# Optimization experiments

Measured on AMD Instinct MI355X. Metric: run time of the kernel, lower is better.

Reference implementation:

```python
import jax, jax.numpy as jnp
import numpy as np

N_NODES = 100000


def gcn_conv(x, src, dst, w, W, b, n):
    # PyG GCNConv: add self loops (weight 1), symmetric normalization,
    # linear transform, scatter-add aggregation, bias.
    loop = jnp.arange(n, dtype=src.dtype)
    s = jnp.concatenate([src, loop])
    d = jnp.concatenate([dst, loop])
    ew = jnp.concatenate([w, jnp.ones((n,), dtype=w.dtype)])
    deg = jax.ops.segment_sum(ew, d, num_segments=n)          # [N]
    dinv = jnp.where(deg > 0, jax.lax.rsqrt(deg), 0.0).astype(x.dtype)
    norm = dinv[s] * ew * dinv[d]                             # [E+N]
    h = x @ W                                                 # [N, out]
    msg = h[s] * norm[:, None]                                # gather + scale
    out = jax.ops.segment_sum(msg, d, num_segments=n)         # scatter-add
    return out + b


def setup_inputs() -> dict:
    key = jax.random.key(0)
    k1, k2, k3, k4, k5, k6 = jax.random.split(key, 6)
    n, e, c_in, c_hid, c_out = N_NODES, 1200000, 64, 64, 32
    node_matrix = jax.random.normal(k1, (n, c_in), dtype=jnp.float32)
    edge_index = jax.random.randint(k2, (2, e), 0, n, dtype=jnp.int64)
    edge_weights = jax.random.uniform(k3, (e,), dtype=jnp.float32)
    s_in = 1.0 / np.sqrt(c_in)
    s_hid = 1.0 / np.sqrt(c_hid)
    W1 = jax.random.uniform(k4, (c_in, c_hid), jnp.float32, -s_in, s_in)
    b1 = jnp.zeros((c_hid,), jnp.float32)
    W2 = jax.random.uniform(k5, (c_hid, c_out), jnp.float32, -s_hid, s_hid)
    b2 = jnp.zeros((c_out,), jnp.float32)
    return {"node_matrix": node_matrix, "edge_index": edge_index,
            "edge_weights": edge_weights, "W1": W1, "b1": b1, "W2": W2, "b2": b2}


def reference(node_matrix, edge_index, edge_weights, W1, b1, W2, b2):
    n = node_matrix.shape[0]
    src, dst = edge_index[0], edge_index[1]
    x = gcn_conv(node_matrix, src, dst, edge_weights, W1, b1, n)
    x = jax.nn.relu(x)
    x = gcn_conv(x, src, dst, edge_weights, W2, b2, n)
    return x
```

## Files before the change

kernel.cpp:

```cpp
#include <hip/hip_runtime.h>

static inline int ceil_div(long long a, long long b) { return (int)((a + b - 1) / b); }

#define RBITS 8
#define RNODES 256
#define CNT_BLOCKS 96

typedef __attribute__((ext_vector_type(8))) short bf16x8;
typedef __attribute__((ext_vector_type(4))) float f32x4;

__device__ inline unsigned f2bf(float f) {
    unsigned u = __float_as_uint(f);
    return (u + 0x7fffu + ((u >> 16) & 1u)) >> 16;
}
__device__ inline unsigned pack2(float a, float b) { return f2bf(a) | (f2bf(b) << 16); }
__device__ inline float bf2f(unsigned v) { return __uint_as_float(v << 16); }
__device__ inline float bf_lo(unsigned v) { return __uint_as_float(v << 16); }
__device__ inline float bf_hi(unsigned v) { return __uint_as_float(v & 0xffff0000u); }

__global__ void bin_count(const int* __restrict__ dst, int* __restrict__ hist_g,
                          int NB, int E) {
    __shared__ int hist[512];
    int t = threadIdx.x;
    hist[t] = 0;
    __syncthreads();
    int nvec = E >> 2;
    const int4* d4 = (const int4*)dst;
    for (int v = blockIdx.x * 512 + t; v < nvec; v += CNT_BLOCKS * 512) {
        int4 d = d4[v];
        atomicAdd(&hist[d.x >> RBITS], 1);
        atomicAdd(&hist[d.y >> RBITS], 1);
        atomicAdd(&hist[d.z >> RBITS], 1);
        atomicAdd(&hist[d.w >> RBITS], 1);
    }
    if (blockIdx.x == 0 && t < (E & 3))
        atomicAdd(&hist[dst[(nvec << 2) + t] >> RBITS], 1);
    __syncthreads();
    if (t < NB) hist_g[blockIdx.x * NB + t] = hist[t];
}

__global__ void bin_scan(const int* __restrict__ hist_g, int* __restrict__ bin_start,
                         int* __restrict__ bin_cursor, int NB) {
    __shared__ int s[512];
    int t = threadIdx.x;
    int v = 0;
    if (t < NB) {
        for (int k = 0; k < CNT_BLOCKS; ++k) v += hist_g[k * NB + t];
        bin_cursor[t] = 0;
    }
    s[t] = v;
    __syncthreads();
    for (int d = 1; d < 512; d <<= 1) {
        int a = (t >= d) ? s[t - d] : 0;
        __syncthreads();
        s[t] += a;
        __syncthreads();
    }
    if (t < NB) bin_start[t] = s[t] - v;
    if (t == NB - 1) bin_start[NB] = s[t];
}

#define SC_T 512
#define SC_K 8
#define SC_E (SC_T * SC_K)
__global__ void bin_scatter(const int* __restrict__ src, const int* __restrict__ dst,
                            const float* __restrict__ w, int* __restrict__ bin_cursor,
                            const int* __restrict__ bin_start,
                            int* __restrict__ bp, float* __restrict__ bw,
                            int NB, int E) {
    __shared__ int hist[512];
    __shared__ int offs[512];
    __shared__ int base[512];
    __shared__ int stage_p[SC_E];
    __shared__ float stage_w[SC_E];
    __shared__ unsigned short stage_b[SC_E];
    int t = threadIdx.x;
    hist[t] = 0;
    __syncthreads();
    int e0 = blockIdx.x * SC_E;
    int nE = E - e0; if (nE > SC_E) nE = SC_E;

    int myBin[SC_K], myRank[SC_K], myPack[SC_K];
    float myW[SC_K];
#pragma unroll
    for (int k = 0; k < SC_K; ++k) {
        int idx = t + k * SC_T;
        if (idx < nE) {
            int e = e0 + idx;
            int d = dst[e];
            int b = d >> RBITS;
            myBin[k] = b;
            myPack[k] = (src[e] << RBITS) | (d & (RNODES - 1));
            myW[k] = w[e];
            myRank[k] = atomicAdd(&hist[b], 1);
        }
    }
    __syncthreads();
    offs[t] = hist[t];
    __syncthreads();
    for (int d = 1; d < 512; d <<= 1) {
        int a = (t >= d) ? offs[t - d] : 0;
        __syncthreads();
        offs[t] += a;
        __syncthreads();
    }
    if (t < NB && hist[t]) base[t] = bin_start[t] + atomicAdd(&bin_cursor[t], hist[t]);
#pragma unroll
    for (int k = 0; k < SC_K; ++k) {
        int idx = t + k * SC_T;
        if (idx < nE) {
            int b = myBin[k];
            int pos = (offs[b] - hist[b]) + myRank[k];
            stage_p[pos] = myPack[k];
            stage_w[pos] = myW[k];
            stage_b[pos] = (unsigned short)b;
        }
    }
    __syncthreads();
    for (int p = t; p < nE; p += SC_T) {
        int b = stage_b[p];
        int g = base[b] + (p - (offs[b] - hist[b]));
        bp[g] = stage_p[p];
        bw[g] = stage_w[p];
    }
}

__global__ void deg_csr(const int* __restrict__ bp, const float* __restrict__ bw,
                        const int* __restrict__ bin_start,
                        int* __restrict__ row_beg, int* __restrict__ row_cnt,
                        float* __restrict__ dinv, int N) {
    __shared__ int cnt[RNODES];
    __shared__ float wsum[RNODES];
    __shared__ int starts[RNODES];
    int b = blockIdx.x;
    int t = threadIdx.x;
    if (t < RNODES) { cnt[t] = 0; wsum[t] = 0.f; }
    __syncthreads();
    int beg = bin_start[b], end = bin_start[b + 1];
    for (int e = beg + t; e < end; e += 512) {
        int off = bp[e] & (RNODES - 1);
        atomicAdd(&cnt[off], 1);
        atomicAdd(&wsum[off], bw[e]);
    }
    __syncthreads();
    if (t < RNODES) starts[t] = cnt[t];
    __syncthreads();
    for (int d = 1; d < RNODES; d <<= 1) {
        int a = 0;
        if (t < RNODES && t >= d) a = starts[t - d];
        __syncthreads();
        if (t < RNODES) starts[t] += a;
        __syncthreads();
    }
    if (t < RNODES) {
        int node = (b << RBITS) + t;
        if (node < N) {
            row_beg[node] = beg + (starts[t] - cnt[t]);
            row_cnt[node] = cnt[t];
            dinv[node] = rsqrtf(wsum[t] + 1.0f);
        }
    }
}

__global__ void csr_scatter(const int* __restrict__ bp, const float* __restrict__ bw,
                            const int* __restrict__ bin_start, const int* __restrict__ row_beg,
                            const float* __restrict__ dinv, uint2* __restrict__ ew, int N) {
    __shared__ int cur[RNODES];
    int b = blockIdx.x;
    int t = threadIdx.x;
    if (t < RNODES) {
        int node = (b << RBITS) + t;
        cur[t] = (node < N) ? row_beg[node] : 0;
    }
    __syncthreads();
    int beg = bin_start[b], end = bin_start[b + 1];
    for (int e = beg + t; e < end; e += 512) {
        int p = bp[e];
        int s = p >> RBITS;
        int slot = atomicAdd(&cur[p & (RNODES - 1)], 1);
        uint2 v;
        v.x = (unsigned)s;
        v.y = __float_as_uint(bw[e] * dinv[s]);
        ew[slot] = v;
    }
}

__global__ __launch_bounds__(256) void gemm1_mfma(const float* __restrict__ X,
                                                  const float* __restrict__ W,
                                                  unsigned short* __restrict__ H, int N) {
    int lane = threadIdx.x & 63;
    int wv = threadIdx.x >> 6;
    int quad = lane >> 4;
    int col = lane & 15;

    bf16x8 Bh[4][2], Bl[4][2];
#pragma unroll
    for (int nt = 0; nt < 4; ++nt)
#pragma unroll
        for (int kh = 0; kh < 2; ++kh)
#pragma unroll
            for (int j = 0; j < 8; ++j) {
                float wval = W[(kh * 32 + quad * 8 + j) * 64 + nt * 16 + col];
                unsigned hb = f2bf(wval);
                Bh[nt][kh][j] = (short)hb;
                Bl[nt][kh][j] = (short)f2bf(wval - bf2f(hb));
            }

#pragma unroll
    for (int rt = 0; rt < 4; ++rt) {
        int rb = blockIdx.x * 256 + wv * 64 + rt * 16;
        if (rb >= N) break;
        int arow = rb + col;
        bf16x8 Ah[2], Al[2];
#pragma unroll
        for (int kh = 0; kh < 2; ++kh) {
            float xv[8];
            if (arow < N) {
                const float4* p = (const float4*)(X + (size_t)arow * 64 + kh * 32 + quad * 8);
                float4 f0 = p[0], f1 = p[1];
                xv[0] = f0.x; xv[1] = f0.y; xv[2] = f0.z; xv[3] = f0.w;
                xv[4] = f1.x; xv[5] = f1.y; xv[6] = f1.z; xv[7] = f1.w;
            } else {
#pragma unroll
                for (int j = 0; j < 8; ++j) xv[j] = 0.f;
            }
#pragma unroll
            for (int j = 0; j < 8; ++j) {
                unsigned hb = f2bf(xv[j]);
                Ah[kh][j] = (short)hb;
                Al[kh][j] = (short)f2bf(xv[j] - bf2f(hb));
            }
        }
        f32x4 acc[4] = {{0,0,0,0},{0,0,0,0},{0,0,0,0},{0,0,0,0}};
#pragma unroll
        for (int nt = 0; nt < 4; ++nt)
#pragma unroll
            for (int kh = 0; kh < 2; ++kh) {
                acc[nt] = __builtin_amdgcn_mfma_f32_16x16x32_bf16(Ah[kh], Bh[nt][kh], acc[nt], 0, 0, 0);
                acc[nt] = __builtin_amdgcn_mfma_f32_16x16x32_bf16(Al[kh], Bh[nt][kh], acc[nt], 0, 0, 0);
                acc[nt] = __builtin_amdgcn_mfma_f32_16x16x32_bf16(Ah[kh], Bl[nt][kh], acc[nt], 0, 0, 0);
            }
#pragma unroll
        for (int nt = 0; nt < 4; ++nt)
#pragma unroll
            for (int r = 0; r < 4; ++r) {
                int row = rb + quad * 4 + r;
                if (row < N)
                    H[(size_t)row * 64 + nt * 16 + col] = (unsigned short)f2bf(acc[nt][r]);
            }
    }
}

__global__ __launch_bounds__(256) void gemm2_mfma(const unsigned short* __restrict__ Xb,
                                                  const float* __restrict__ W,
                                                  unsigned short* __restrict__ H, int N) {
    int lane = threadIdx.x & 63;
    int wv = threadIdx.x >> 6;
    int quad = lane >> 4;
    int col = lane & 15;

    bf16x8 Bh[2][2], Bl[2][2];
#pragma unroll
    for (int nt = 0; nt < 2; ++nt)
#pragma unroll
        for (int kh = 0; kh < 2; ++kh)
#pragma unroll
            for (int j = 0; j < 8; ++j) {
                float wval = W[(kh * 32 + quad * 8 + j) * 32 + nt * 16 + col];
                unsigned hb = f2bf(wval);
                Bh[nt][kh][j] = (short)hb;
                Bl[nt][kh][j] = (short)f2bf(wval - bf2f(hb));
            }

#pragma unroll
    for (int rt = 0; rt < 4; ++rt) {
        int rb = blockIdx.x * 256 + wv * 64 + rt * 16;
        if (rb >= N) break;
        int arow = rb + col;
        bf16x8 A[2];
#pragma unroll
        for (int kh = 0; kh < 2; ++kh) {
            if (arow < N) {
                const bf16x8* p = (const bf16x8*)(Xb + (size_t)arow * 64 + kh * 32 + quad * 8);
                A[kh] = *p;
            } else {
                A[kh] = bf16x8{0,0,0,0,0,0,0,0};
            }
        }
        f32x4 acc[2] = {{0,0,0,0},{0,0,0,0}};
#pragma unroll
        for (int nt = 0; nt < 2; ++nt)
#pragma unroll
            for (int kh = 0; kh < 2; ++kh) {
                acc[nt] = __builtin_amdgcn_mfma_f32_16x16x32_bf16(A[kh], Bh[nt][kh], acc[nt], 0, 0, 0);
                acc[nt] = __builtin_amdgcn_mfma_f32_16x16x32_bf16(A[kh], Bl[nt][kh], acc[nt], 0, 0, 0);
            }
#pragma unroll
        for (int nt = 0; nt < 2; ++nt)
#pragma unroll
            for (int r = 0; r < 4; ++r) {
                int row = rb + quad * 4 + r;
                if (row < N)
                    H[(size_t)row * 32 + nt * 16 + col] = (unsigned short)f2bf(acc[nt][r]);
            }
    }
}

__global__ void aggregate64(const unsigned* __restrict__ h, const int* __restrict__ row_beg,
                            const int* __restrict__ row_cnt, const uint2* __restrict__ ew,
                            const float* __restrict__ dinv, const float* __restrict__ b,
                            unsigned* __restrict__ outb, int N) {
    int t = threadIdx.x;
    int c = t & 7;
    int i = blockIdx.x * 64 + (t >> 3);
    if (i >= N) return;
    int e = row_beg[i];
    int end = e + row_cnt[i];
    const uint4* h4 = (const uint4*)h;
    float acc[8];
#pragma unroll
    for (int j = 0; j < 8; ++j) acc[j] = 0.f;
    for (; e + 3 < end; e += 4) {
        uint2 e0 = ew[e], e1 = ew[e + 1], e2 = ew[e + 2], e3 = ew[e + 3];
        float n0 = __uint_as_float(e0.y);
        float n1 = __uint_as_float(e1.y);
        float n2 = __uint_as_float(e2.y);
        float n3 = __uint_as_float(e3.y);
        uint4 v0 = h4[(size_t)e0.x * 8 + c];
        uint4 v1 = h4[(size_t)e1.x * 8 + c];
        uint4 v2 = h4[(size_t)e2.x * 8 + c];
        uint4 v3 = h4[(size_t)e3.x * 8 + c];
        acc[0] += n0 * bf_lo(v0.x) + n1 * bf_lo(v1.x) + n2 * bf_lo(v2.x) + n3 * bf_lo(v3.x);
        acc[1] += n0 * bf_hi(v0.x) + n1 * bf_hi(v1.x) + n2 * bf_hi(v2.x) + n3 * bf_hi(v3.x);
        acc[2] += n0 * bf_lo(v0.y) + n1 * bf_lo(v1.y) + n2 * bf_lo(v2.y) + n3 * bf_lo(v3.y);
        acc[3] += n0 * bf_hi(v0.y) + n1 * bf_hi(v1.y) + n2 * bf_hi(v2.y) + n3 * bf_hi(v3.y);
        acc[4] += n0 * bf_lo(v0.z) + n1 * bf_lo(v1.z) + n2 * bf_lo(v2.z) + n3 * bf_lo(v3.z);
        acc[5] += n0 * bf_hi(v0.z) + n1 * bf_hi(v1.z) + n2 * bf_hi(v2.z) + n3 * bf_hi(v3.z);
        acc[6] += n0 * bf_lo(v0.w) + n1 * bf_lo(v1.w) + n2 * bf_lo(v2.w) + n3 * bf_lo(v3.w);
        acc[7] += n0 * bf_hi(v0.w) + n1 * bf_hi(v1.w) + n2 * bf_hi(v2.w) + n3 * bf_hi(v3.w);
    }
    for (; e < end; ++e) {
        uint2 e0 = ew[e];
        float n0 = __uint_as_float(e0.y);
        uint4 v0 = h4[(size_t)e0.x * 8 + c];
        acc[0] += n0 * bf_lo(v0.x);
        acc[1] += n0 * bf_hi(v0.x);
        acc[2] += n0 * bf_lo(v0.y);
        acc[3] += n0 * bf_hi(v0.y);
        acc[4] += n0 * bf_lo(v0.z);
        acc[5] += n0 * bf_hi(v0.z);
        acc[6] += n0 * bf_lo(v0.w);
        acc[7] += n0 * bf_hi(v0.w);
    }
    float di = dinv[i];
    uint4 hv = h4[(size_t)i * 8 + c];
    float hs[8] = {bf_lo(hv.x), bf_hi(hv.x), bf_lo(hv.y), bf_hi(hv.y),
                   bf_lo(hv.z), bf_hi(hv.z), bf_lo(hv.w), bf_hi(hv.w)};
    float4 b0 = ((const float4*)b)[c * 2];
    float4 b1 = ((const float4*)b)[c * 2 + 1];
    float o[8];
    o[0] = b0.x + di * (di * hs[0] + acc[0]);
    o[1] = b0.y + di * (di * hs[1] + acc[1]);
    o[2] = b0.z + di * (di * hs[2] + acc[2]);
    o[3] = b0.w + di * (di * hs[3] + acc[3]);
    o[4] = b1.x + di * (di * hs[4] + acc[4]);
    o[5] = b1.y + di * (di * hs[5] + acc[5]);
    o[6] = b1.z + di * (di * hs[6] + acc[6]);
    o[7] = b1.w + di * (di * hs[7] + acc[7]);
#pragma unroll
    for (int j = 0; j < 8; ++j) o[j] = fmaxf(o[j], 0.f);
    uint4 ov;
    ov.x = pack2(o[0], o[1]);
    ov.y = pack2(o[2], o[3]);
    ov.z = pack2(o[4], o[5]);
    ov.w = pack2(o[6], o[7]);
    ((uint4*)outb)[(size_t)i * 8 + c] = ov;
}

__global__ void aggregate32(const unsigned* __restrict__ h, const int* __restrict__ row_beg,
                            const int* __restrict__ row_cnt, const uint2* __restrict__ ew,
                            const float* __restrict__ dinv, const float* __restrict__ b,
                            float* __restrict__ out, int N) {
    int t = threadIdx.x;
    int c = t & 3;
    int i = blockIdx.x * 128 + (t >> 2);
    if (i >= N) return;
    int e = row_beg[i];
    int end = e + row_cnt[i];
    const uint4* h4 = (const uint4*)h;
    float acc[8];
#pragma unroll
    for (int j = 0; j < 8; ++j) acc[j] = 0.f;
    for (; e + 3 < end; e += 4) {
        uint2 e0 = ew[e], e1 = ew[e + 1], e2 = ew[e + 2], e3 = ew[e + 3];
        float n0 = __uint_as_float(e0.y);
        float n1 = __uint_as_float(e1.y);
        float n2 = __uint_as_float(e2.y);
        float n3 = __uint_as_float(e3.y);
        uint4 v0 = h4[(size_t)e0.x * 4 + c];
        uint4 v1 = h4[(size_t)e1.x * 4 + c];
        uint4 v2 = h4[(size_t)e2.x * 4 + c];
        uint4 v3 = h4[(size_t)e3.x * 4 + c];
        acc[0] += n0 * bf_lo(v0.x) + n1 * bf_lo(v1.x) + n2 * bf_lo(v2.x) + n3 * bf_lo(v3.x);
        acc[1] += n0 * bf_hi(v0.x) + n1 * bf_hi(v1.x) + n2 * bf_hi(v2.x) + n3 * bf_hi(v3.x);
        acc[2] += n0 * bf_lo(v0.y) + n1 * bf_lo(v1.y) + n2 * bf_lo(v2.y) + n3 * bf_lo(v3.y);
        acc[3] += n0 * bf_hi(v0.y) + n1 * bf_hi(v1.y) + n2 * bf_hi(v2.y) + n3 * bf_hi(v3.y);
        acc[4] += n0 * bf_lo(v0.z) + n1 * bf_lo(v1.z) + n2 * bf_lo(v2.z) + n3 * bf_lo(v3.z);
        acc[5] += n0 * bf_hi(v0.z) + n1 * bf_hi(v1.z) + n2 * bf_hi(v2.z) + n3 * bf_hi(v3.z);
        acc[6] += n0 * bf_lo(v0.w) + n1 * bf_lo(v1.w) + n2 * bf_lo(v2.w) + n3 * bf_lo(v3.w);
        acc[7] += n0 * bf_hi(v0.w) + n1 * bf_hi(v1.w) + n2 * bf_hi(v2.w) + n3 * bf_hi(v3.w);
    }
    for (; e < end; ++e) {
        uint2 e0 = ew[e];
        float n0 = __uint_as_float(e0.y);
        uint4 v0 = h4[(size_t)e0.x * 4 + c];
        acc[0] += n0 * bf_lo(v0.x);
        acc[1] += n0 * bf_hi(v0.x);
        acc[2] += n0 * bf_lo(v0.y);
        acc[3] += n0 * bf_hi(v0.y);
        acc[4] += n0 * bf_lo(v0.z);
        acc[5] += n0 * bf_hi(v0.z);
        acc[6] += n0 * bf_lo(v0.w);
        acc[7] += n0 * bf_hi(v0.w);
    }
    float di = dinv[i];
    uint4 hv = h4[(size_t)i * 4 + c];
    float hs[8] = {bf_lo(hv.x), bf_hi(hv.x), bf_lo(hv.y), bf_hi(hv.y),
                   bf_lo(hv.z), bf_hi(hv.z), bf_lo(hv.w), bf_hi(hv.w)};
    float4 b0 = ((const float4*)b)[c * 2];
    float4 b1 = ((const float4*)b)[c * 2 + 1];
    float4 o0, o1;
    o0.x = b0.x + di * (di * hs[0] + acc[0]);
    o0.y = b0.y + di * (di * hs[1] + acc[1]);
    o0.z = b0.z + di * (di * hs[2] + acc[2]);
    o0.w = b0.w + di * (di * hs[3] + acc[3]);
    o1.x = b1.x + di * (di * hs[4] + acc[4]);
    o1.y = b1.y + di * (di * hs[5] + acc[5]);
    o1.z = b1.z + di * (di * hs[6] + acc[6]);
    o1.w = b1.w + di * (di * hs[7] + acc[7]);
    float4* op = (float4*)(out + (size_t)i * 32 + c * 8);
    op[0] = o0;
    op[1] = o1;
}

extern "C" void kernel_launch(void* const* d_in, const int* in_sizes, int n_in,
                              void* d_out, int out_size, void* d_ws, size_t ws_size,
                              hipStream_t stream) {
    const float* x  = (const float*)d_in[0];
    const int* eidx = (const int*)d_in[1];
    const float* w  = (const float*)d_in[2];
    const float* W1 = (const float*)d_in[3];
    const float* b1 = (const float*)d_in[4];
    const float* W2 = (const float*)d_in[5];
    const float* b2 = (const float*)d_in[6];
    float* out = (float*)d_out;

    const int E = in_sizes[2];
    const int N = in_sizes[0] / 64;
    const int* src = eidx;
    const int* dst = eidx + E;
    const int NB = ceil_div(N, RNODES);

    char* ws = (char*)d_ws;
    size_t off = 0;
    auto alloc = [&](size_t bytes) -> void* {
        void* p = ws + off;
        off = (off + bytes + 255) & ~(size_t)255;
        return p;
    };
    int*      hist_g     = (int*)alloc((size_t)CNT_BLOCKS * NB * 4);
    int*      bin_cursor = (int*)alloc((size_t)NB * 4);
    int*      bin_start  = (int*)alloc((size_t)(NB + 1) * 4);
    int*      bp         = (int*)alloc((size_t)E * 4);
    float*    bw         = (float*)alloc((size_t)E * 4);
    uint2*    ew         = (uint2*)alloc((size_t)E * 8);
    int*      row_beg    = (int*)alloc((size_t)N * 4);
    int*      row_cnt    = (int*)alloc((size_t)N * 4);
    float*    dinv       = (float*)alloc((size_t)N * 4);
    unsigned* h1         = (unsigned*)alloc((size_t)N * 32 * 4);
    unsigned* out1b      = (unsigned*)alloc((size_t)N * 32 * 4);
    unsigned* h2         = (unsigned*)alloc((size_t)N * 16 * 4);

    bin_count<<<CNT_BLOCKS, 512, 0, stream>>>(dst, hist_g, NB, E);
    bin_scan<<<1, 512, 0, stream>>>(hist_g, bin_start, bin_cursor, NB);
    bin_scatter<<<ceil_div(E, SC_E), SC_T, 0, stream>>>(src, dst, w, bin_cursor, bin_start,
                                                        bp, bw, NB, E);
    deg_csr<<<NB, 512, 0, stream>>>(bp, bw, bin_start, row_beg, row_cnt, dinv, N);
    csr_scatter<<<NB, 512, 0, stream>>>(bp, bw, bin_start, row_beg, dinv, ew, N);

    gemm1_mfma<<<ceil_div(N, 256), 256, 0, stream>>>(x, W1, (unsigned short*)h1, N);
    aggregate64<<<ceil_div(N, 64), 512, 0, stream>>>(h1, row_beg, row_cnt, ew, dinv, b1, out1b, N);

    gemm2_mfma<<<ceil_div(N, 256), 256, 0, stream>>>((const unsigned short*)out1b, W2,
                                                     (unsigned short*)h2, N);
    aggregate32<<<ceil_div(N, 128), 512, 0, stream>>>(h2, row_beg, row_cnt, ew, dinv, b2, out, N);
}
```

Before: 201.9 us.

## Fold source dinv into GEMM output, pack edges to 4 bytes, merge CSR kernels

The source-side degree normalization now happens in the GEMM epilogue (h scaled by dinv per row). Each CSR edge entry then only needs the raw weight, packed with the source index into one 32-bit word (17-bit index, 15-bit bf16 weight). The degree/CSR-offset kernel and the CSR scatter kernel are merged into one, staging the bin's edges in shared memory so they are read from global memory once. This halves edge-list traffic in both aggregation passes and drops a launch. In exchange, edge weights lose precision to truncated bf16 and node indices are limited to 17 bits.

```diff
diff --git a/kernel.cpp b/kernel.cpp
--- a/kernel.cpp
+++ b/kernel.cpp
@@ -5,6 +5,7 @@
 #define RBITS 8
 #define RNODES 256
 #define CNT_BLOCKS 96
+#define STAGE_CAP 4096
 
 typedef __attribute__((ext_vector_type(8))) short bf16x8;
 typedef __attribute__((ext_vector_type(4))) float f32x4;
@@ -125,22 +126,28 @@
     }
 }
 
-__global__ void deg_csr(const int* __restrict__ bp, const float* __restrict__ bw,
-                        const int* __restrict__ bin_start,
-                        int* __restrict__ row_beg, int* __restrict__ row_cnt,
-                        float* __restrict__ dinv, int N) {
+__global__ void csr_build(const int* __restrict__ bp, const float* __restrict__ bw,
+                          const int* __restrict__ bin_start,
+                          int* __restrict__ row_beg, int* __restrict__ row_cnt,
+                          float* __restrict__ dinv, unsigned* __restrict__ ew, int N) {
     __shared__ int cnt[RNODES];
     __shared__ float wsum[RNODES];
     __shared__ int starts[RNODES];
+    __shared__ int cur[RNODES];
+    __shared__ int sp[STAGE_CAP];
+    __shared__ float sw[STAGE_CAP];
     int b = blockIdx.x;
     int t = threadIdx.x;
     if (t < RNODES) { cnt[t] = 0; wsum[t] = 0.f; }
     __syncthreads();
     int beg = bin_start[b], end = bin_start[b + 1];
-    for (int e = beg + t; e < end; e += 512) {
-        int off = bp[e] & (RNODES - 1);
-        atomicAdd(&cnt[off], 1);
-        atomicAdd(&wsum[off], bw[e]);
+    int n = end - beg;
+    for (int idx = t; idx < n; idx += 512) {
+        int p = bp[beg + idx];
+        float wv = bw[beg + idx];
+        if (idx < STAGE_CAP) { sp[idx] = p; sw[idx] = wv; }
+        atomicAdd(&cnt[p & (RNODES - 1)], 1);
+        atomicAdd(&wsum[p & (RNODES - 1)], wv);
     }
     __syncthreads();
     if (t < RNODES) starts[t] = cnt[t];
@@ -153,40 +160,29 @@
         __syncthreads();
     }
     if (t < RNODES) {
+        int ex = starts[t] - cnt[t];
+        cur[t] = beg + ex;
         int node = (b << RBITS) + t;
         if (node < N) {
-            row_beg[node] = beg + (starts[t] - cnt[t]);
+            row_beg[node] = beg + ex;
             row_cnt[node] = cnt[t];
             dinv[node] = rsqrtf(wsum[t] + 1.0f);
         }
     }
-}
-
-__global__ void csr_scatter(const int* __restrict__ bp, const float* __restrict__ bw,
-                            const int* __restrict__ bin_start, const int* __restrict__ row_beg,
-                            const float* __restrict__ dinv, uint2* __restrict__ ew, int N) {
-    __shared__ int cur[RNODES];
-    int b = blockIdx.x;
-    int t = threadIdx.x;
-    if (t < RNODES) {
-        int node = (b << RBITS) + t;
-        cur[t] = (node < N) ? row_beg[node] : 0;
-    }
-    __syncthreads();
-    int beg = bin_start[b], end = bin_start[b + 1];
-    for (int e = beg + t; e < end; e += 512) {
-        int p = bp[e];
-        int s = p >> RBITS;
+    __syncthreads();
+    for (int idx = t; idx < n; idx += 512) {
+        int p;
+        float wv;
+        if (idx < STAGE_CAP) { p = sp[idx]; wv = sw[idx]; }
+        else { p = bp[beg + idx]; wv = bw[beg + idx]; }
         int slot = atomicAdd(&cur[p & (RNODES - 1)], 1);
-        uint2 v;
-        v.x = (unsigned)s;
-        v.y = __float_as_uint(bw[e] * dinv[s]);
-        ew[slot] = v;
+        ew[slot] = ((unsigned)(p >> RBITS) << 15) | (f2bf(wv) & 0x7fffu);
     }
 }
 
 __global__ __launch_bounds__(256) void gemm1_mfma(const float* __restrict__ X,
                                                   const float* __restrict__ W,
+                                                  const float* __restrict__ dinv,
                                                   unsigned short* __restrict__ H, int N) {
     int lane = threadIdx.x & 63;
     int wv = threadIdx.x >> 6;
@@ -240,19 +236,26 @@
                 acc[nt] = __builtin_amdgcn_mfma_f32_16x16x32_bf16(Al[kh], Bh[nt][kh], acc[nt], 0, 0, 0);
                 acc[nt] = __builtin_amdgcn_mfma_f32_16x16x32_bf16(Ah[kh], Bl[nt][kh], acc[nt], 0, 0, 0);
             }
+        float dval[4];
+#pragma unroll
+        for (int r = 0; r < 4; ++r) {
+            int row = rb + quad * 4 + r;
+            dval[r] = (row < N) ? dinv[row] : 0.f;
+        }
 #pragma unroll
         for (int nt = 0; nt < 4; ++nt)
 #pragma unroll
             for (int r = 0; r < 4; ++r) {
                 int row = rb + quad * 4 + r;
                 if (row < N)
-                    H[(size_t)row * 64 + nt * 16 + col] = (unsigned short)f2bf(acc[nt][r]);
+                    H[(size_t)row * 64 + nt * 16 + col] = (unsigned short)f2bf(acc[nt][r] * dval[r]);
             }
     }
 }
 
 __global__ __launch_bounds__(256) void gemm2_mfma(const unsigned short* __restrict__ Xb,
                                                   const float* __restrict__ W,
+                                                  const float* __restrict__ dinv,
                                                   unsigned short* __restrict__ H, int N) {
     int lane = threadIdx.x & 63;
     int wv = threadIdx.x >> 6;
@@ -295,19 +298,25 @@
                 acc[nt] = __builtin_amdgcn_mfma_f32_16x16x32_bf16(A[kh], Bh[nt][kh], acc[nt], 0, 0, 0);
                 acc[nt] = __builtin_amdgcn_mfma_f32_16x16x32_bf16(A[kh], Bl[nt][kh], acc[nt], 0, 0, 0);
             }
+        float dval[4];
+#pragma unroll
+        for (int r = 0; r < 4; ++r) {
+            int row = rb + quad * 4 + r;
+            dval[r] = (row < N) ? dinv[row] : 0.f;
+        }
 #pragma unroll
         for (int nt = 0; nt < 2; ++nt)
 #pragma unroll
             for (int r = 0; r < 4; ++r) {
                 int row = rb + quad * 4 + r;
                 if (row < N)
-                    H[(size_t)row * 32 + nt * 16 + col] = (unsigned short)f2bf(acc[nt][r]);
-            }
-    }
-}
-
-__global__ void aggregate64(const unsigned* __restrict__ h, const int* __restrict__ row_beg,
-                            const int* __restrict__ row_cnt, const uint2* __restrict__ ew,
+                    H[(size_t)row * 32 + nt * 16 + col] = (unsigned short)f2bf(acc[nt][r] * dval[r]);
+            }
+    }
+}
+
+__global__ void aggregate64(const unsigned* __restrict__ g, const int* __restrict__ row_beg,
+                            const int* __restrict__ row_cnt, const unsigned* __restrict__ ew,
                             const float* __restrict__ dinv, const float* __restrict__ b,
                             unsigned* __restrict__ outb, int N) {
     int t = threadIdx.x;
@@ -316,20 +325,20 @@
     if (i >= N) return;
     int e = row_beg[i];
     int end = e + row_cnt[i];
-    const uint4* h4 = (const uint4*)h;
+    const uint4* h4 = (const uint4*)g;
     float acc[8];
 #pragma unroll
     for (int j = 0; j < 8; ++j) acc[j] = 0.f;
     for (; e + 3 < end; e += 4) {
-        uint2 e0 = ew[e], e1 = ew[e + 1], e2 = ew[e + 2], e3 = ew[e + 3];
-        float n0 = __uint_as_float(e0.y);
-        float n1 = __uint_as_float(e1.y);
-        float n2 = __uint_as_float(e2.y);
-        float n3 = __uint_as_float(e3.y);
-        uint4 v0 = h4[(size_t)e0.x * 8 + c];
-        uint4 v1 = h4[(size_t)e1.x * 8 + c];
-        uint4 v2 = h4[(size_t)e2.x * 8 + c];
-        uint4 v3 = h4[(size_t)e3.x * 8 + c];
+        unsigned e0 = ew[e], e1 = ew[e + 1], e2 = ew[e + 2], e3 = ew[e + 3];
+        float n0 = __uint_as_float((e0 & 0x7fffu) << 16);
+        float n1 = __uint_as_float((e1 & 0x7fffu) << 16);
+        float n2 = __uint_as_float((e2 & 0x7fffu) << 16);
+        float n3 = __uint_as_float((e3 & 0x7fffu) << 16);
+        uint4 v0 = h4[(size_t)(e0 >> 15) * 8 + c];
+        uint4 v1 = h4[(size_t)(e1 >> 15) * 8 + c];
+        uint4 v2 = h4[(size_t)(e2 >> 15) * 8 + c];
+        uint4 v3 = h4[(size_t)(e3 >> 15) * 8 + c];
         acc[0] += n0 * bf_lo(v0.x) + n1 * bf_lo(v1.x) + n2 * bf_lo(v2.x) + n3 * bf_lo(v3.x);
         acc[1] += n0 * bf_hi(v0.x) + n1 * bf_hi(v1.x) + n2 * bf_hi(v2.x) + n3 * bf_hi(v3.x);
         acc[2] += n0 * bf_lo(v0.y) + n1 * bf_lo(v1.y) + n2 * bf_lo(v2.y) + n3 * bf_lo(v3.y);
@@ -340,9 +349,9 @@
         acc[7] += n0 * bf_hi(v0.w) + n1 * bf_hi(v1.w) + n2 * bf_hi(v2.w) + n3 * bf_hi(v3.w);
     }
     for (; e < end; ++e) {
-        uint2 e0 = ew[e];
-        float n0 = __uint_as_float(e0.y);
-        uint4 v0 = h4[(size_t)e0.x * 8 + c];
+        unsigned e0 = ew[e];
+        float n0 = __uint_as_float((e0 & 0x7fffu) << 16);
+        uint4 v0 = h4[(size_t)(e0 >> 15) * 8 + c];
         acc[0] += n0 * bf_lo(v0.x);
         acc[1] += n0 * bf_hi(v0.x);
         acc[2] += n0 * bf_lo(v0.y);
@@ -359,14 +368,14 @@
     float4 b0 = ((const float4*)b)[c * 2];
     float4 b1 = ((const float4*)b)[c * 2 + 1];
     float o[8];
-    o[0] = b0.x + di * (di * hs[0] + acc[0]);
-    o[1] = b0.y + di * (di * hs[1] + acc[1]);
-    o[2] = b0.z + di * (di * hs[2] + acc[2]);
-    o[3] = b0.w + di * (di * hs[3] + acc[3]);
-    o[4] = b1.x + di * (di * hs[4] + acc[4]);
-    o[5] = b1.y + di * (di * hs[5] + acc[5]);
-    o[6] = b1.z + di * (di * hs[6] + acc[6]);
-    o[7] = b1.w + di * (di * hs[7] + acc[7]);
+    o[0] = b0.x + di * (hs[0] + acc[0]);
+    o[1] = b0.y + di * (hs[1] + acc[1]);
+    o[2] = b0.z + di * (hs[2] + acc[2]);
+    o[3] = b0.w + di * (hs[3] + acc[3]);
+    o[4] = b1.x + di * (hs[4] + acc[4]);
+    o[5] = b1.y + di * (hs[5] + acc[5]);
+    o[6] = b1.z + di * (hs[6] + acc[6]);
+    o[7] = b1.w + di * (hs[7] + acc[7]);
 #pragma unroll
     for (int j = 0; j < 8; ++j) o[j] = fmaxf(o[j], 0.f);
     uint4 ov;
@@ -377,8 +386,8 @@
     ((uint4*)outb)[(size_t)i * 8 + c] = ov;
 }
 
-__global__ void aggregate32(const unsigned* __restrict__ h, const int* __restrict__ row_beg,
-                            const int* __restrict__ row_cnt, const uint2* __restrict__ ew,
+__global__ void aggregate32(const unsigned* __restrict__ g, const int* __restrict__ row_beg,
+                            const int* __restrict__ row_cnt, const unsigned* __restrict__ ew,
                             const float* __restrict__ dinv, const float* __restrict__ b,
                             float* __restrict__ out, int N) {
     int t = threadIdx.x;
@@ -387,20 +396,20 @@
     if (i >= N) return;
     int e = row_beg[i];
     int end = e + row_cnt[i];
-    const uint4* h4 = (const uint4*)h;
+    const uint4* h4 = (const uint4*)g;
     float acc[8];
 #pragma unroll
     for (int j = 0; j < 8; ++j) acc[j] = 0.f;
     for (; e + 3 < end; e += 4) {
-        uint2 e0 = ew[e], e1 = ew[e + 1], e2 = ew[e + 2], e3 = ew[e + 3];
-        float n0 = __uint_as_float(e0.y);
-        float n1 = __uint_as_float(e1.y);
-        float n2 = __uint_as_float(e2.y);
-        float n3 = __uint_as_float(e3.y);
-        uint4 v0 = h4[(size_t)e0.x * 4 + c];
-        uint4 v1 = h4[(size_t)e1.x * 4 + c];
-        uint4 v2 = h4[(size_t)e2.x * 4 + c];
-        uint4 v3 = h4[(size_t)e3.x * 4 + c];
+        unsigned e0 = ew[e], e1 = ew[e + 1], e2 = ew[e + 2], e3 = ew[e + 3];
+        float n0 = __uint_as_float((e0 & 0x7fffu) << 16);
+        float n1 = __uint_as_float((e1 & 0x7fffu) << 16);
+        float n2 = __uint_as_float((e2 & 0x7fffu) << 16);
+        float n3 = __uint_as_float((e3 & 0x7fffu) << 16);
+        uint4 v0 = h4[(size_t)(e0 >> 15) * 4 + c];
+        uint4 v1 = h4[(size_t)(e1 >> 15) * 4 + c];
+        uint4 v2 = h4[(size_t)(e2 >> 15) * 4 + c];
+        uint4 v3 = h4[(size_t)(e3 >> 15) * 4 + c];
         acc[0] += n0 * bf_lo(v0.x) + n1 * bf_lo(v1.x) + n2 * bf_lo(v2.x) + n3 * bf_lo(v3.x);
         acc[1] += n0 * bf_hi(v0.x) + n1 * bf_hi(v1.x) + n2 * bf_hi(v2.x) + n3 * bf_hi(v3.x);
         acc[2] += n0 * bf_lo(v0.y) + n1 * bf_lo(v1.y) + n2 * bf_lo(v2.y) + n3 * bf_lo(v3.y);
@@ -411,9 +420,9 @@
         acc[7] += n0 * bf_hi(v0.w) + n1 * bf_hi(v1.w) + n2 * bf_hi(v2.w) + n3 * bf_hi(v3.w);
     }
     for (; e < end; ++e) {
-        uint2 e0 = ew[e];
-        float n0 = __uint_as_float(e0.y);
-        uint4 v0 = h4[(size_t)e0.x * 4 + c];
+        unsigned e0 = ew[e];
+        float n0 = __uint_as_float((e0 & 0x7fffu) << 16);
+        uint4 v0 = h4[(size_t)(e0 >> 15) * 4 + c];
         acc[0] += n0 * bf_lo(v0.x);
         acc[1] += n0 * bf_hi(v0.x);
         acc[2] += n0 * bf_lo(v0.y);
@@ -430,14 +439,14 @@
     float4 b0 = ((const float4*)b)[c * 2];
     float4 b1 = ((const float4*)b)[c * 2 + 1];
     float4 o0, o1;
-    o0.x = b0.x + di * (di * hs[0] + acc[0]);
-    o0.y = b0.y + di * (di * hs[1] + acc[1]);
-    o0.z = b0.z + di * (di * hs[2] + acc[2]);
-    o0.w = b0.w + di * (di * hs[3] + acc[3]);
-    o1.x = b1.x + di * (di * hs[4] + acc[4]);
-    o1.y = b1.y + di * (di * hs[5] + acc[5]);
-    o1.z = b1.z + di * (di * hs[6] + acc[6]);
-    o1.w = b1.w + di * (di * hs[7] + acc[7]);
+    o0.x = b0.x + di * (hs[0] + acc[0]);
+    o0.y = b0.y + di * (hs[1] + acc[1]);
+    o0.z = b0.z + di * (hs[2] + acc[2]);
+    o0.w = b0.w + di * (hs[3] + acc[3]);
+    o1.x = b1.x + di * (hs[4] + acc[4]);
+    o1.y = b1.y + di * (hs[5] + acc[5]);
+    o1.z = b1.z + di * (hs[6] + acc[6]);
+    o1.w = b1.w + di * (hs[7] + acc[7]);
     float4* op = (float4*)(out + (size_t)i * 32 + c * 8);
     op[0] = o0;
     op[1] = o1;
@@ -473,25 +482,24 @@
     int*      bin_start  = (int*)alloc((size_t)(NB + 1) * 4);
     int*      bp         = (int*)alloc((size_t)E * 4);
     float*    bw         = (float*)alloc((size_t)E * 4);
-    uint2*    ew         = (uint2*)alloc((size_t)E * 8);
+    unsigned* ew         = (unsigned*)alloc((size_t)E * 4);
     int*      row_beg    = (int*)alloc((size_t)N * 4);
     int*      row_cnt    = (int*)alloc((size_t)N * 4);
     float*    dinv       = (float*)alloc((size_t)N * 4);
-    unsigned* h1         = (unsigned*)alloc((size_t)N * 32 * 4);
+    unsigned* g1         = (unsigned*)alloc((size_t)N * 32 * 4);
     unsigned* out1b      = (unsigned*)alloc((size_t)N * 32 * 4);
-    unsigned* h2         = (unsigned*)alloc((size_t)N * 16 * 4);
+    unsigned* g2         = (unsigned*)alloc((size_t)N * 16 * 4);
 
     bin_count<<<CNT_BLOCKS, 512, 0, stream>>>(dst, hist_g, NB, E);
     bin_scan<<<1, 512, 0, stream>>>(hist_g, bin_start, bin_cursor, NB);
     bin_scatter<<<ceil_div(E, SC_E), SC_T, 0, stream>>>(src, dst, w, bin_cursor, bin_start,
                                                         bp, bw, NB, E);
-    deg_csr<<<NB, 512, 0, stream>>>(bp, bw, bin_start, row_beg, row_cnt, dinv, N);
-    csr_scatter<<<NB, 512, 0, stream>>>(bp, bw, bin_start, row_beg, dinv, ew, N);
-
-    gemm1_mfma<<<ceil_div(N, 256), 256, 0, stream>>>(x, W1, (unsigned short*)h1, N);
-    aggregate64<<<ceil_div(N, 64), 512, 0, stream>>>(h1, row_beg, row_cnt, ew, dinv, b1, out1b, N);
-
-    gemm2_mfma<<<ceil_div(N, 256), 256, 0, stream>>>((const unsigned short*)out1b, W2,
-                                                     (unsigned short*)h2, N);
-    aggregate32<<<ceil_div(N, 128), 512, 0, stream>>>(h2, row_beg, row_cnt, ew, dinv, b2, out, N);
-}
+    csr_build<<<NB, 512, 0, stream>>>(bp, bw, bin_start, row_beg, row_cnt, dinv, ew, N);
+
+    gemm1_mfma<<<ceil_div(N, 256), 256, 0, stream>>>(x, W1, dinv, (unsigned short*)g1, N);
+    aggregate64<<<ceil_div(N, 64), 512, 0, stream>>>(g1, row_beg, row_cnt, ew, dinv, b1, out1b, N);
+
+    gemm2_mfma<<<ceil_div(N, 256), 256, 0, stream>>>((const unsigned short*)out1b, W2, dinv,
+                                                     (unsigned short*)g2, N);
+    aggregate32<<<ceil_div(N, 128), 512, 0, stream>>>(g2, row_beg, row_cnt, ew, dinv, b2, out, N);
+}
```

Result: no change. 204.3 us (+1.2%).
